# Optimization experiments

Hardware: AMD Instinct MI355X
Metric: run time of the kernel (lower is better)

The kernel has to match this reference:

```python
import jax, jax.numpy as jnp
import numpy as np

K = 1024  # number of superpixels (spx.max()+1 in the original)

def setup_inputs() -> dict:
    key = jax.random.key(0)
    k1, k2 = jax.random.split(key)
    img = jax.random.normal(k1, (4, 128, 512, 512), dtype=jnp.float32)
    spx = jax.random.randint(k2, (4, 512, 512), 0, K, dtype=jnp.int32)
    return {"img": img, "spx": spx}

def _segment_max_one(img_b, spx_b):
    # img_b: [C, H, W], spx_b: [H, W]
    C = img_b.shape[0]
    data = img_b.reshape(C, -1).T          # [HW, C]
    ids = spx_b.reshape(-1)                # [HW]
    out = jax.ops.segment_max(data, ids, num_segments=K)  # [K, C]
    return out.T                           # [C, K]

def reference(img, spx):
    # Max-pool features over superpixel segments: output [B, C, K]
    return jax.vmap(_segment_max_one)(img, spx)
```

## Files before the change

kernel.cpp:

```cpp
#include <hip/hip_runtime.h>

#define KSEG   1024
#define CCH    128
#define HWPIX  (512 * 512)
#define BB     4
#define CG     8
#define BLOCK  256
#define PIX_PER_BLOCK 16384
#define ITERS  (PIX_PER_BLOCK / (BLOCK * 4))

#define ORD_NEG_INF ((int)0x807FFFFF)

__device__ __forceinline__ int ord_f32(float f) {
    int i = __float_as_int(f);
    return i >= 0 ? i : (i ^ 0x7FFFFFFF);
}

__global__ __launch_bounds__(BLOCK) void init_kernel(int* __restrict__ out) {
    out[blockIdx.x * BLOCK + threadIdx.x] = ORD_NEG_INF;
}

__global__ __launch_bounds__(BLOCK) void decode_kernel(int* __restrict__ out) {
    const int idx = blockIdx.x * BLOCK + threadIdx.x;
    const int i = out[idx];
    ((float*)out)[idx] = __int_as_float(i >= 0 ? i : (i ^ 0x7FFFFFFF));
}

__global__ __launch_bounds__(BLOCK) void pool_kernel(const float* __restrict__ img,
                                                     const int* __restrict__ spx,
                                                     int* __restrict__ out) {
    __shared__ int lmax[CG * KSEG];
    for (int i = threadIdx.x; i < CG * KSEG; i += BLOCK) lmax[i] = ORD_NEG_INF;
    __syncthreads();

    const int b  = blockIdx.z;
    const int c0 = blockIdx.y * CG;
    const int* __restrict__ spx_b = spx + b * HWPIX;
    const float* __restrict__ img_b = img + ((size_t)(b * CCH + c0)) * HWPIX;

    int p = blockIdx.x * PIX_PER_BLOCK + threadIdx.x * 4;
    for (int it = 0; it < ITERS; ++it, p += BLOCK * 4) {
        const int4 id = *(const int4*)(spx_b + p);
#pragma unroll
        for (int j = 0; j < CG; ++j) {
            const float4 v = *(const float4*)(img_b + (size_t)j * HWPIX + p);
            atomicMax(&lmax[j * KSEG + id.x], ord_f32(v.x));
            atomicMax(&lmax[j * KSEG + id.y], ord_f32(v.y));
            atomicMax(&lmax[j * KSEG + id.z], ord_f32(v.z));
            atomicMax(&lmax[j * KSEG + id.w], ord_f32(v.w));
        }
    }
    __syncthreads();

    for (int i = threadIdx.x; i < CG * KSEG; i += BLOCK) {
        const int j = i >> 10;
        const int k = i & (KSEG - 1);
        atomicMax(&out[((size_t)(b * CCH + c0 + j)) * KSEG + k], lmax[i]);
    }
}

extern "C" void kernel_launch(void* const* d_in, const int* in_sizes, int n_in,
                              void* d_out, int out_size, void* d_ws, size_t ws_size,
                              hipStream_t stream) {
    const float* img = (const float*)d_in[0];
    const int*   spx = (const int*)d_in[1];
    int* out = (int*)d_out;

    init_kernel<<<out_size / BLOCK, BLOCK, 0, stream>>>(out);

    dim3 grid(HWPIX / PIX_PER_BLOCK, CCH / CG, BB);
    pool_kernel<<<grid, BLOCK, 0, stream>>>(img, spx, out);

    decode_kernel<<<out_size / BLOCK, BLOCK, 0, stream>>>(out);
}
```

Before: 704.5 us.

## Replace shared-memory atomic max with per-window counting sort and segment gather

Each block now bucket-sorts the pixel indices of an 8192-pixel window by superpixel id, using a shared-memory histogram, a block-wide prefix scan and a scatter. It then reuses that sort across 32 channels: each thread owns four segments and reduces them serially by gathering values from a staged channel buffer, with the next channel prefetched into registers. This is meant to remove the heavy contention of per-pixel shared atomicMax calls. In exchange it adds sort overhead, irregular shared-memory gathers, load imbalance across segments, and high register use for the prefetch array.

After: 804.6 us. 14.2% more time.

```diff
diff --git a/kernel.cpp b/kernel.cpp
--- a/kernel.cpp
+++ b/kernel.cpp
@@ -4,10 +4,10 @@
 #define CCH    128
 #define HWPIX  (512 * 512)
 #define BB     4
-#define CG     8
 #define BLOCK  256
-#define PIX_PER_BLOCK 16384
-#define ITERS  (PIX_PER_BLOCK / (BLOCK * 4))
+#define W      8192
+#define CGRP   32
+#define LITERS (W / (BLOCK * 4))
 
 #define ORD_NEG_INF ((int)0x807FFFFF)
 
@@ -29,33 +29,103 @@
 __global__ __launch_bounds__(BLOCK) void pool_kernel(const float* __restrict__ img,
                                                      const int* __restrict__ spx,
                                                      int* __restrict__ out) {
-    __shared__ int lmax[CG * KSEG];
-    for (int i = threadIdx.x; i < CG * KSEG; i += BLOCK) lmax[i] = ORD_NEG_INF;
+    __shared__ unsigned short sidx[W];
+    __shared__ int start[KSEG + 1];
+    __shared__ int cursor[KSEG];
+    __shared__ __align__(16) float buf[W];
+    __shared__ int scanbuf[BLOCK];
+
+    const int tid = threadIdx.x;
+    const int b   = blockIdx.z;
+    const int c0  = blockIdx.y * CGRP;
+    const int wx  = blockIdx.x * W;
+    const int* __restrict__ spx_w = spx + b * HWPIX + wx;
+    const float* __restrict__ img_w = img + ((size_t)(b * CCH + c0)) * HWPIX + wx;
+
+    for (int i = tid; i < KSEG; i += BLOCK) cursor[i] = 0;
     __syncthreads();
 
-    const int b  = blockIdx.z;
-    const int c0 = blockIdx.y * CG;
-    const int* __restrict__ spx_b = spx + b * HWPIX;
-    const float* __restrict__ img_b = img + ((size_t)(b * CCH + c0)) * HWPIX;
-
-    int p = blockIdx.x * PIX_PER_BLOCK + threadIdx.x * 4;
-    for (int it = 0; it < ITERS; ++it, p += BLOCK * 4) {
-        const int4 id = *(const int4*)(spx_b + p);
-#pragma unroll
-        for (int j = 0; j < CG; ++j) {
-            const float4 v = *(const float4*)(img_b + (size_t)j * HWPIX + p);
-            atomicMax(&lmax[j * KSEG + id.x], ord_f32(v.x));
-            atomicMax(&lmax[j * KSEG + id.y], ord_f32(v.y));
-            atomicMax(&lmax[j * KSEG + id.z], ord_f32(v.z));
-            atomicMax(&lmax[j * KSEG + id.w], ord_f32(v.w));
-        }
+    for (int it = 0; it < LITERS; ++it) {
+        const int4 id = *(const int4*)(spx_w + (it * BLOCK + tid) * 4);
+        atomicAdd(&cursor[id.x], 1);
+        atomicAdd(&cursor[id.y], 1);
+        atomicAdd(&cursor[id.z], 1);
+        atomicAdd(&cursor[id.w], 1);
     }
     __syncthreads();
 
-    for (int i = threadIdx.x; i < CG * KSEG; i += BLOCK) {
-        const int j = i >> 10;
-        const int k = i & (KSEG - 1);
-        atomicMax(&out[((size_t)(b * CCH + c0 + j)) * KSEG + k], lmax[i]);
+    int loc[4], s0 = 0;
+#pragma unroll
+    for (int j = 0; j < 4; ++j) { loc[j] = s0; s0 += cursor[tid * 4 + j]; }
+    scanbuf[tid] = s0;
+    __syncthreads();
+    for (int off = 1; off < BLOCK; off <<= 1) {
+        const int v = (tid >= off) ? scanbuf[tid - off] : 0;
+        __syncthreads();
+        scanbuf[tid] += v;
+        __syncthreads();
+    }
+    const int base = scanbuf[tid] - s0;
+#pragma unroll
+    for (int j = 0; j < 4; ++j) {
+        start[tid * 4 + j]  = base + loc[j];
+        cursor[tid * 4 + j] = base + loc[j];
+    }
+    if (tid == 0) start[KSEG] = W;
+    __syncthreads();
+
+    for (int it = 0; it < LITERS; ++it) {
+        const int p = (it * BLOCK + tid) * 4;
+        const int4 id = *(const int4*)(spx_w + p);
+        sidx[atomicAdd(&cursor[id.x], 1)] = (unsigned short)(p);
+        sidx[atomicAdd(&cursor[id.y], 1)] = (unsigned short)(p + 1);
+        sidx[atomicAdd(&cursor[id.z], 1)] = (unsigned short)(p + 2);
+        sidx[atomicAdd(&cursor[id.w], 1)] = (unsigned short)(p + 3);
+    }
+    __syncthreads();
+
+    int rs[4], re[4];
+#pragma unroll
+    for (int q = 0; q < 4; ++q) {
+        rs[q] = start[tid + q * BLOCK];
+        re[q] = start[tid + q * BLOCK + 1];
+    }
+
+    const float NEG_INF = __int_as_float(0xFF800000);
+
+    float4 r[LITERS];
+#pragma unroll
+    for (int it = 0; it < LITERS; ++it)
+        r[it] = *(const float4*)(img_w + (size_t)0 * HWPIX + (it * BLOCK + tid) * 4);
+
+    for (int c = 0; c < CGRP; ++c) {
+        __syncthreads();
+#pragma unroll
+        for (int it = 0; it < LITERS; ++it)
+            *(float4*)&buf[(it * BLOCK + tid) * 4] = r[it];
+        if (c + 1 < CGRP) {
+            const float* __restrict__ src = img_w + (size_t)(c + 1) * HWPIX;
+#pragma unroll
+            for (int it = 0; it < LITERS; ++it)
+                r[it] = *(const float4*)(src + (it * BLOCK + tid) * 4);
+        }
+        __syncthreads();
+
+        int* __restrict__ outc = out + ((size_t)(b * CCH + c0 + c)) * KSEG;
+#pragma unroll
+        for (int q = 0; q < 4; ++q) {
+            const int s = tid + q * BLOCK;
+            float m = NEG_INF;
+            int i = rs[q];
+            const int e = re[q];
+            for (; i + 4 <= e; i += 4) {
+                const int i0 = sidx[i], i1 = sidx[i + 1], i2 = sidx[i + 2], i3 = sidx[i + 3];
+                const float a = buf[i0], bb2 = buf[i1], cc = buf[i2], dd = buf[i3];
+                m = fmaxf(m, fmaxf(fmaxf(a, bb2), fmaxf(cc, dd)));
+            }
+            for (; i < e; ++i) m = fmaxf(m, buf[sidx[i]]);
+            atomicMax(&outc[s], ord_f32(m));
+        }
     }
 }
 
@@ -68,7 +138,7 @@
 
     init_kernel<<<out_size / BLOCK, BLOCK, 0, stream>>>(out);
 
-    dim3 grid(HWPIX / PIX_PER_BLOCK, CCH / CG, BB);
+    dim3 grid(HWPIX / W, CCH / CGRP, BB);
     pool_kernel<<<grid, BLOCK, 0, stream>>>(img, spx, out);
 
     decode_kernel<<<out_size / BLOCK, BLOCK, 0, stream>>>(out);
```
